# Performance work log

Measured on AMD Instinct MI355X. Metric: run time of the kernel, lower is better.

The kernel has to match this reference:

```python
import jax, jax.numpy as jnp
import numpy as np

B, S, D, H, L, DZ, POI, MAXP = 128, 512, 128, 4, 4, 128, 50000, 32
HD = D // H
EPS_LN = 1e-5

def layernorm(x, g, b):
    m = x.mean(-1, keepdims=True)
    v = ((x - m) ** 2).mean(-1, keepdims=True)
    return (x - m) * jax.lax.rsqrt(v + EPS_LN) * g + b

def setup_inputs() -> dict:
    key = jax.random.key(0)
    ks = iter(jax.random.split(key, 48))
    r = lambda shp, s=0.05: jax.random.normal(next(ks), shp, jnp.float32) * s
    return dict(
        d_t=jax.random.uniform(next(ks), (B, S), jnp.float32),
        d_l=jax.random.normal(next(ks), (B, S, 2), jnp.float32),
        d_emb=jax.random.randint(next(ks), (B, S), 0, POI),
        d_pad=jnp.zeros((B, S + 1), bool),
        num_pred=jax.random.randint(next(ks), (B,), 1, MAXP + 1),
        poi_table=r((POI, D), 0.02),
        W_time=r((D, 1)), W_space=r((D, 2)),
        agg_token=r((1, 1, D)),
        Wqkv=r((L, 3 * D, D), D ** -0.5), bqkv=jnp.zeros((L, 3 * D)),
        Wo=r((L, D, D), D ** -0.5), bo=jnp.zeros((L, D)),
        ln1_g=jnp.ones((L, D)), ln1_b=jnp.zeros((L, D)),
        W1=r((L, 2 * D, D), D ** -0.5), b1=jnp.zeros((L, 2 * D)),
        W2=r((L, D, 2 * D), (2 * D) ** -0.5), b2=jnp.zeros((L, D)),
        ln2_g=jnp.ones((L, D)), ln2_b=jnp.zeros((L, D)),
        Wg=r((DZ, D)), bg=jnp.zeros((DZ,)),
        Wt=r((DZ, D)), bt=jnp.zeros((DZ,)),
        gru_Wih=r((3 * D, D)), gru_Whh=r((3 * D, D)),
        gru_bih=jnp.zeros((3 * D,)), gru_bhh=jnp.zeros((3 * D,)),
        Wfc=r((1, D)), bfc=jnp.zeros((1,)),
    )

def reference(d_t, d_l, d_emb, d_pad, num_pred, poi_table, W_time, W_space, agg_token,
              Wqkv, bqkv, Wo, bo, ln1_g, ln1_b, W1, b1, W2, b2, ln2_g, ln2_b,
              Wg, bg, Wt, bt, gru_Wih, gru_Whh, gru_bih, gru_bhh, Wfc, bfc):
    # ---- Encoder: fused time/space/poi embeddings + agg token -> post-norm transformer stack ----
    t_emb = jnp.einsum('bs,d->bsd', d_t, W_time[:, 0])          # Linear(1, D, bias=False)
    c_emb = jnp.einsum('bsc,dc->bsd', d_l, W_space)             # Linear(2, D, bias=False)
    p_emb = poi_table[d_emb]                                    # [B,S,D]
    x = jnp.concatenate([t_emb + c_emb + p_emb,
                         jnp.broadcast_to(agg_token, (x_shape := (B, 1, D)))], axis=1)  # [B,S+1,D]
    T = S + 1
    neg = jnp.finfo(x.dtype).min
    for i in range(L):  # structurally distinct layers (post-norm, ReLU FFN, dropout=0)
        qkv = x @ Wqkv[i].T + bqkv[i]
        q, k, v = jnp.split(qkv, 3, axis=-1)
        hsplit = lambda t: t.reshape(B, T, H, HD).transpose(0, 2, 1, 3)
        q, k, v = hsplit(q), hsplit(k), hsplit(v)
        scores = jnp.einsum('bhqd,bhkd->bhqk', q, k) / jnp.sqrt(jnp.asarray(HD, x.dtype))
        scores = jnp.where(d_pad[:, None, None, :], neg, scores)
        attn = jax.nn.softmax(scores, axis=-1)
        o = jnp.einsum('bhqk,bhkd->bhqd', attn, v).transpose(0, 2, 1, 3).reshape(B, T, D)
        x = layernorm(x + o @ Wo[i].T + bo[i], ln1_g[i], ln1_b[i])
        ff = jax.nn.relu(x @ W1[i].T + b1[i]) @ W2[i].T + b2[i]
        x = layernorm(x + ff, ln2_g[i], ln2_b[i])
    ctx = x[:, -1, :]                                           # agg-token summary [B,D]
    gamma = ctx @ Wg.T + bg
    tau = jax.nn.softplus(ctx @ Wt.T + bt)

    # ---- DynamicTimeGenerator: batched GRUCell recurrence (input is the fixed zero init token) ----
    gi = jnp.zeros((1, D), ctx.dtype) @ gru_Wih.T + gru_bih      # [1,3D] input-side gates (x == 0)
    def step(h, _):
        gh = h @ gru_Whh.T + gru_bhh
        r = jax.nn.sigmoid(gi[:, :D] + gh[:, :D])
        z = jax.nn.sigmoid(gi[:, D:2 * D] + gh[:, D:2 * D])
        n = jnp.tanh(gi[:, 2 * D:] + r * gh[:, 2 * D:])
        h_new = (1.0 - z) * n + z * h
        delta = jax.nn.softplus(h_new @ Wfc.T + bfc)[:, 0]       # [B]
        return h_new, delta
    _, deltas = jax.lax.scan(step, ctx, None, length=MAXP)       # [MAXP, B]
    cum = jnp.cumsum(deltas, axis=0).T                           # [B, MAXP]
    last = jnp.take_along_axis(cum, (num_pred - 1)[:, None], axis=1)
    normed = cum / (last + 1e-6)
    valid = jnp.arange(MAXP)[None, :] < num_pred[:, None]
    times = jnp.zeros((B, MAXP + 2), ctx.dtype).at[:, 1:MAXP + 1].set(jnp.where(valid, normed, 0.0))
    times = times + jax.nn.one_hot(num_pred + 1, MAXP + 2, dtype=ctx.dtype)  # trailing 1.0 sentinel

    # ---- KL(q(z1)=N(gamma, tau^2) || N(0, I)) per kl_norm_norm ----
    a = jnp.sum(tau ** 2, -1, keepdims=True)
    b = jnp.sum(gamma ** 2, -1, keepdims=True)
    c = -2.0 * jnp.sum(jnp.log(tau), -1, keepdims=True)
    kl = 0.5 * (a + b + c - DZ)

    return jnp.concatenate([times, ctx, gamma, tau, kl], axis=-1)  # [B, MAXP+2+D+2*DZ+1]
```

## Files before the change

kernel.cpp:

```cpp
#include <hip/hip_runtime.h>

#define BB 128
#define SS 512
#define TT 513
#define DD 128
#define HH 4
#define LL 4
#define MM (BB*TT)

typedef __attribute__((ext_vector_type(4))) float f32x4;
typedef __attribute__((ext_vector_type(16))) float f32x16;
typedef __attribute__((ext_vector_type(8))) short short8;

__device__ __forceinline__ float b2f(ushort u){
  union { uint i; float f; } c; c.i = ((uint)u) << 16; return c.f;
}
__device__ __forceinline__ ushort f2b(float f){
  union { float f; uint i; } c; c.f = f;
  uint x = c.i;
  return (ushort)((x + 0x7fffu + ((x >> 16) & 1u)) >> 16);
}
union S8 { short8 v; ushort u[8]; };

__device__ __forceinline__ uint cvtpk(float lo, float hi){
  uint r;
  asm("v_cvt_pk_bf16_f32 %0, %1, %2" : "=v"(r) : "v"(lo), "v"(hi));
  return r;
}
__device__ __forceinline__ float fexp2(float x){
#if __has_builtin(__builtin_amdgcn_exp2f)
  return __builtin_amdgcn_exp2f(x);
#else
  return exp2f(x);
#endif
}

__global__ __launch_bounds__(256) void k_embed(
    const float* __restrict__ d_t, const float* __restrict__ d_l, const int* __restrict__ d_emb,
    const float* __restrict__ poi, const float* __restrict__ W_time, const float* __restrict__ W_space,
    const float* __restrict__ agg, ushort* __restrict__ xb)
{
  int gid = blockIdx.x*256 + threadIdx.x;
  if (gid >= MM*DD) return;
  int d = gid & 127;
  int m = gid >> 7;
  int b = m / TT, t = m % TT;
  float v;
  if (t == SS) v = agg[d];
  else {
    int bs = b*SS + t;
    v = d_t[bs]*W_time[d] + d_l[bs*2]*W_space[d*2] + d_l[bs*2+1]*W_space[d*2+1]
        + poi[(size_t)d_emb[bs]*DD + d];
  }
  xb[gid] = f2b(v);
}

__global__ __launch_bounds__(256) void k_f2b(const float* __restrict__ src, ushort* __restrict__ dst, int n){
  int i = blockIdx.x*256 + threadIdx.x;
  if (i < n) dst[i] = f2b(src[i]);
}

template<bool RELU, bool OUTB>
__global__ __launch_bounds__(256) void k_gemm(
  const ushort* __restrict__ A, const ushort* __restrict__ W,
  const float* __restrict__ bias, void* __restrict__ Cout,
  const int N, const int K)
{
  __shared__ __align__(16) ushort As[64*128], Ws[64*128];
  const int tid = threadIdx.x;
  const int m0 = blockIdx.x * 64, n0 = blockIdx.y * 64;
  const int l = tid & 63, wid = tid >> 6;
  const int wr = wid >> 1, wc = wid & 1;
  const int lr = l & 15, lg = l >> 4;
  f32x4 acc[2][2] = {};
  for (int kt = 0; kt < K; kt += 128){
    if (kt) __syncthreads();
    for (int i = tid; i < 1024; i += 256){
      const int row = i >> 4, ch = i & 15;
      const int bo_ = (ch*16) ^ ((row & 7) << 4);
      *(short8*)((char*)As + row*256 + bo_) = *(const short8*)&A[(size_t)(m0+row)*K + kt + ch*8];
      *(short8*)((char*)Ws + row*256 + bo_) = *(const short8*)&W[(size_t)(n0+row)*K + kt + ch*8];
    }
    __syncthreads();
    #pragma unroll
    for (int k0 = 0; k0 < 128; k0 += 32){
      const int sw = ((k0 + lg*8)*2) ^ ((lr & 7) << 4);
      short8 a0 = *(const short8*)((const char*)As + (wr*32+lr)*256 + sw);
      short8 a1 = *(const short8*)((const char*)As + (wr*32+16+lr)*256 + sw);
      short8 b0 = *(const short8*)((const char*)Ws + (wc*32+lr)*256 + sw);
      short8 b1 = *(const short8*)((const char*)Ws + (wc*32+16+lr)*256 + sw);
      acc[0][0] = __builtin_amdgcn_mfma_f32_16x16x32_bf16(a0, b0, acc[0][0], 0,0,0);
      acc[0][1] = __builtin_amdgcn_mfma_f32_16x16x32_bf16(a0, b1, acc[0][1], 0,0,0);
      acc[1][0] = __builtin_amdgcn_mfma_f32_16x16x32_bf16(a1, b0, acc[1][0], 0,0,0);
      acc[1][1] = __builtin_amdgcn_mfma_f32_16x16x32_bf16(a1, b1, acc[1][1], 0,0,0);
    }
  }
  #pragma unroll
  for (int i=0;i<2;i++)
  #pragma unroll
  for (int j=0;j<2;j++)
  #pragma unroll
  for (int r=0;r<4;r++){
    const int lm = wr*32 + i*16 + lg*4 + r;
    const int ln = wc*32 + j*16 + lr;
    const size_t idx = (size_t)(m0+lm)*N + (n0+ln);
    float v = acc[i][j][r] + bias[n0+ln];
    if (RELU) v = fmaxf(v, 0.f);
    if (OUTB) ((ushort*)Cout)[idx] = f2b(v);
    else ((float*)Cout)[idx] = v;
  }
}

__global__ __launch_bounds__(256) void k_gemm_ln(
  const ushort* __restrict__ A, const ushort* __restrict__ W,
  const float* __restrict__ bias, ushort* __restrict__ xb,
  const float* __restrict__ g, const float* __restrict__ bb, const int K)
{
  __shared__ __align__(16) ushort As[64*128], Ws[128*128];
  const int tid = threadIdx.x;
  const int m0 = blockIdx.x * 64;
  const int l = tid & 63, w = tid >> 6;
  const int lr = l & 15, lg = l >> 4;
  f32x4 acc[8] = {};
  for (int kt = 0; kt < K; kt += 128){
    if (kt) __syncthreads();
    for (int i = tid; i < 1024; i += 256){
      const int row = i >> 4, ch = i & 15;
      const int bo_ = (ch*16) ^ ((row & 7) << 4);
      *(short8*)((char*)As + row*256 + bo_) = *(const short8*)&A[(size_t)(m0+row)*K + kt + ch*8];
    }
    for (int i = tid; i < 2048; i += 256){
      const int row = i >> 4, ch = i & 15;
      const int bo_ = (ch*16) ^ ((row & 7) << 4);
      *(short8*)((char*)Ws + row*256 + bo_) = *(const short8*)&W[(size_t)row*K + kt + ch*8];
    }
    __syncthreads();
    #pragma unroll
    for (int k0 = 0; k0 < 128; k0 += 32){
      const int sw = ((k0 + lg*8)*2) ^ ((lr & 7) << 4);
      short8 a = *(const short8*)((const char*)As + (w*16+lr)*256 + sw);
      #pragma unroll
      for (int j=0;j<8;j++){
        short8 bf = *(const short8*)((const char*)Ws + (j*16+lr)*256 + sw);
        acc[j] = __builtin_amdgcn_mfma_f32_16x16x32_bf16(a, bf, acc[j], 0,0,0);
      }
    }
  }
  float biasj[8], gj[8], bj[8];
  #pragma unroll
  for (int j=0;j<8;j++){ biasj[j]=bias[j*16+lr]; gj[j]=g[j*16+lr]; bj[j]=bb[j*16+lr]; }
  #pragma unroll
  for (int r=0;r<4;r++){
    const size_t row = (size_t)(m0 + w*16 + lg*4 + r);
    float resid[8], s=0.f, sq=0.f;
    #pragma unroll
    for (int j=0;j<8;j++){
      float v = acc[j][r] + biasj[j];
      resid[j] = b2f(xb[row*128 + j*16 + lr]) + v;
      s += resid[j]; sq += resid[j]*resid[j];
    }
    #pragma unroll
    for (int off=1; off<16; off<<=1){ s += __shfl_xor(s,off,64); sq += __shfl_xor(sq,off,64); }
    const float mean = s*(1.f/128.f);
    const float var  = fmaxf(sq*(1.f/128.f) - mean*mean, 0.f);
    const float rstd = rsqrtf(var + 1e-5f);
    #pragma unroll
    for (int j=0;j<8;j++){
      float o = (resid[j]-mean)*rstd*gj[j] + bj[j];
      xb[row*128 + j*16 + lr] = f2b(o);
    }
  }
}

#define VSTRIDE 544
#define NEGM 30000.f
#define MFMA32(a,b,c) __builtin_amdgcn_mfma_f32_32x32x16_bf16(a,b,c,0,0,0)

__global__ __launch_bounds__(512) void k_attn(const ushort* __restrict__ qkv, ushort* __restrict__ ao)
{
  __shared__ __align__(16) ushort KL[VSTRIDE*32];
  __shared__ __align__(16) ushort VT[32*VSTRIDE];
  const int tid = threadIdx.x;
  const int b = blockIdx.x >> 2, h = blockIdx.x & 3;
  const size_t base = (size_t)b*TT*384 + h*32;
  union { short4 v; ushort u[4]; } sv;
  for (int i = tid; i < 8*VSTRIDE; i += 512){
    int t = i >> 3, dc = (i & 7)*4;
    sv.u[0]=0; sv.u[1]=0; sv.u[2]=0; sv.u[3]=0;
    if (t < TT) sv.v = *(const short4*)&qkv[base + (size_t)t*384 + 128 + dc];
    *(short4*)((char*)KL + ((t*64 + dc*2) ^ ((t&7)<<4))) = sv.v;
  }
  for (int i = tid; i < 8*VSTRIDE; i += 512){
    int t = i >> 3, dc = (i & 7)*4;
    sv.u[0]=0; sv.u[1]=0; sv.u[2]=0; sv.u[3]=0;
    if (t < TT) sv.v = *(const short4*)&qkv[base + (size_t)t*384 + 256 + dc];
    #pragma unroll
    for (int e=0;e<4;e++){
      int d = dc + e;
      *(ushort*)((char*)VT + ((d*1088 + t*2) ^ ((d&7)<<4))) = sv.u[e];
    }
  }
  __syncthreads();
  const int l = tid & 63, w = tid >> 6;
  const int lq = l & 31, hi = l >> 5;
  const float qscale = 0.25503486341f;
  const int krow = (lq & 3) | ((lq & 4) << 1) | ((lq & 8) >> 1) | (lq & 16);
  f32x16 cinit;
  #pragma unroll
  for (int r=0;r<16;r++) cinit[r] = -40.f;

  for (int qi = 0; qi < 3; qi++){
    const int qb = w + qi*8;
    if (qb >= 17) break;
    const int q0 = qb*32;
    int qrow = q0 + lq; if (qrow > SS) qrow = SS;
    S8 qa, qf0, qf1;
    qa.v = *(const short8*)&qkv[base + (size_t)qrow*384 + hi*8];
    #pragma unroll
    for (int j=0;j<8;j++) qf0.u[j] = f2b(b2f(qa.u[j]) * qscale);
    qa.v = *(const short8*)&qkv[base + (size_t)qrow*384 + 16 + hi*8];
    #pragma unroll
    for (int j=0;j<8;j++) qf1.u[j] = f2b(b2f(qa.u[j]) * qscale);

    float rsl = 0.f;
    f32x16 acc = {};
    int t0 = 0;
    for (int kb = 0; kb < 17; kb++, t0 += 32){
      const int trow = t0 + krow;
      short8 kc0 = *(const short8*)((const char*)KL + ((trow*64 + hi*16)      ^ ((trow&7)<<4)));
      short8 kc1 = *(const short8*)((const char*)KL + ((trow*64 + 32 + hi*16) ^ ((trow&7)<<4)));
      f32x16 s = MFMA32(kc0, qf0.v, cinit);
      s = MFMA32(kc1, qf1.v, s);
      if (t0 + 32 > TT){
        #pragma unroll
        for (int r=0;r<16;r++){
          const int key = t0 + (r&7) + 8*hi + 16*(r>>3);
          if (key >= TT) s[r] = -NEGM;
        }
      }
      float p[16];
      #pragma unroll
      for (int r=0;r<16;r++){ p[r] = fexp2(s[r]); rsl += p[r]; }
      union { short8 v; uint u[4]; } pa0, pa1;
      #pragma unroll
      for (int wd=0; wd<4; wd++){
        pa0.u[wd] = cvtpk(p[2*wd],   p[2*wd+1]);
        pa1.u[wd] = cvtpk(p[8+2*wd], p[8+2*wd+1]);
      }
      short8 v0 = *(const short8*)((const char*)VT + (((lq*1088) + (t0 + hi*8)*2)      ^ ((lq&7)<<4)));
      short8 v1 = *(const short8*)((const char*)VT + (((lq*1088) + (t0 + 16 + hi*8)*2) ^ ((lq&7)<<4)));
      acc = MFMA32(v0, pa0.v, acc);
      acc = MFMA32(v1, pa1.v, acc);
    }
    rsl += __shfl_xor(rsl, 32, 64);
    if (q0 + lq < TT){
      const float inv = 1.f / rsl;
      ushort* orow = ao + ((size_t)(b*TT + q0 + lq))*DD + h*32;
      #pragma unroll
      for (int r=0;r<16;r++){
        const int d = (r&3) + 8*(r>>2) + 4*hi;
        orow[d] = f2b(acc[r]*inv);
      }
    }
  }
}

__global__ __launch_bounds__(256) void k_ctx(
    const ushort* __restrict__ xb, const float* __restrict__ Wg, const float* __restrict__ bg,
    const float* __restrict__ Wt, const float* __restrict__ bt,
    float* __restrict__ out, float* __restrict__ ctxws)
{
  __shared__ float cs[128];
  const int b = blockIdx.x, tid = threadIdx.x;
  const ushort* xr = &xb[((size_t)b*TT + SS)*128];
  if (tid < 128){
    float v = b2f(xr[tid]);
    cs[tid] = v;
    out[(size_t)b*419 + 34 + tid] = v;
    ctxws[b*128 + tid] = v;
  }
  __syncthreads();
  const int j = tid & 127;
  const float* Wrow = (tid < 128) ? &Wg[(size_t)j*128] : &Wt[(size_t)j*128];
  float acc = 0.f;
  #pragma unroll 8
  for (int d=0; d<128; d+=4){
    float4 wv = *(const float4*)&Wrow[d];
    acc += cs[d]*wv.x + cs[d+1]*wv.y + cs[d+2]*wv.z + cs[d+3]*wv.w;
  }
  if (tid < 128){
    out[(size_t)b*419 + 162 + j] = acc + bg[j];
  } else {
    float tv = acc + bt[j];
    float sp = fmaxf(tv, 0.f) + log1pf(__expf(-fabsf(tv)));
    out[(size_t)b*419 + 290 + j] = sp;
  }
}

__global__ __launch_bounds__(384, 1) void k_gru(
    const float* __restrict__ ctx, const float* __restrict__ Whh,
    const float* __restrict__ bih, const float* __restrict__ bhh,
    const float* __restrict__ Wfc, const float* __restrict__ bfc,
    float* __restrict__ deltas)
{
  __shared__ float hs[128], gh[384], red[2];
  const int b = blockIdx.x, tid = threadIdx.x;
  if (tid < 128) hs[tid] = ctx[b*128 + tid];
  float4 wreg[32];
  const float4* wp = (const float4*)&Whh[(size_t)tid*128];
  #pragma unroll
  for (int d=0; d<32; d++) wreg[d] = wp[d];
  const float bhh_t = bhh[tid];
  float bih0=0.f, bih1=0.f, bih2=0.f, wfc_t=0.f;
  if (tid < 128){ bih0=bih[tid]; bih1=bih[128+tid]; bih2=bih[256+tid]; wfc_t=Wfc[tid]; }
  const float bfc0 = bfc[0];
  for (int step=0; step<32; step++){
    __syncthreads();
    float acc = bhh_t;
    #pragma unroll
    for (int d=0; d<32; d++){
      acc += hs[4*d]*wreg[d].x + hs[4*d+1]*wreg[d].y + hs[4*d+2]*wreg[d].z + hs[4*d+3]*wreg[d].w;
    }
    gh[tid] = acc;
    __syncthreads();
    if (tid < 128){
      float r = 1.f/(1.f + __expf(-(bih0 + gh[tid])));
      float z = 1.f/(1.f + __expf(-(bih1 + gh[128+tid])));
      float n = tanhf(bih2 + r*gh[256+tid]);
      float hn = (1.f - z)*n + z*hs[tid];
      hs[tid] = hn;
      float pv = hn * wfc_t;
      #pragma unroll
      for (int off=1; off<64; off<<=1) pv += __shfl_xor(pv, off, 64);
      if ((tid & 63) == 0) red[tid >> 6] = pv;
    }
    __syncthreads();
    if (tid == 0){
      float dv = red[0] + red[1] + bfc0;
      deltas[b*32 + step] = fmaxf(dv, 0.f) + log1pf(__expf(-fabsf(dv)));
    }
  }
}

__global__ __launch_bounds__(64) void k_final(
    const float* __restrict__ deltas, const int* __restrict__ num_pred,
    float* __restrict__ out)
{
  const int b = blockIdx.x, l = threadIdx.x;
  float d = (l < 32) ? deltas[b*32 + l] : 0.f;
  float c = d;
  #pragma unroll
  for (int off=1; off<32; off<<=1){
    float t = __shfl_up(c, off, 64);
    if (l >= off) c += t;
  }
  const int np = num_pred[b];
  float last = __shfl(c, np-1, 64);
  float denom = last + 1e-6f;
  float cjm = __shfl(c, (l==0 ? 0 : l-1), 64);
  float val = 0.f;
  if (l >= 1 && l <= 32 && (l-1) < np) val = cjm / denom;
  if (l == np + 1) val += 1.f;
  if (l < 34) out[(size_t)b*419 + l] = val;
  float ta = 0.f, tb = 0.f, tc = 0.f;
  for (int z = l; z < 128; z += 64){
    float ga = out[(size_t)b*419 + 162 + z];
    float tu = fmaxf(out[(size_t)b*419 + 290 + z], 1e-35f);
    ta += tu*tu; tb += ga*ga; tc += -2.f*logf(tu);
  }
  float v = ta + tb + tc;
  #pragma unroll
  for (int off=1; off<64; off<<=1) v += __shfl_xor(v, off, 64);
  if (l == 0) out[(size_t)b*419 + 418] = 0.5f*(v - 128.f);
}

extern "C" void kernel_launch(void* const* d_in, const int* in_sizes, int n_in,
                              void* d_out, int out_size, void* d_ws, size_t ws_size,
                              hipStream_t stream)
{
  (void)in_sizes; (void)n_in; (void)out_size; (void)ws_size;
  const float* d_t    = (const float*)d_in[0];
  const float* d_l    = (const float*)d_in[1];
  const int*   d_emb  = (const int*)  d_in[2];
  const int*   numprd = (const int*)  d_in[4];
  const float* poi    = (const float*)d_in[5];
  const float* W_time = (const float*)d_in[6];
  const float* W_space= (const float*)d_in[7];
  const float* agg    = (const float*)d_in[8];
  const float* Wqkv   = (const float*)d_in[9];
  const float* bqkv   = (const float*)d_in[10];
  const float* Wo     = (const float*)d_in[11];
  const float* bo     = (const float*)d_in[12];
  const float* ln1g   = (const float*)d_in[13];
  const float* ln1b   = (const float*)d_in[14];
  const float* W1     = (const float*)d_in[15];
  const float* b1     = (const float*)d_in[16];
  const float* W2     = (const float*)d_in[17];
  const float* b2     = (const float*)d_in[18];
  const float* ln2g   = (const float*)d_in[19];
  const float* ln2b   = (const float*)d_in[20];
  const float* Wg     = (const float*)d_in[21];
  const float* bg     = (const float*)d_in[22];
  const float* Wt     = (const float*)d_in[23];
  const float* bt     = (const float*)d_in[24];
  const float* Whh    = (const float*)d_in[26];
  const float* bih    = (const float*)d_in[27];
  const float* bhh    = (const float*)d_in[28];
  const float* Wfc    = (const float*)d_in[29];
  const float* bfc    = (const float*)d_in[30];
  float* out = (float*)d_out;

  char* ws = (char*)d_ws;
  size_t off = 0;
  auto alloc = [&](size_t bytes){ size_t o = off; off += (bytes + 255) & ~(size_t)255; return o; };
  ushort* xb    = (ushort*)(ws + alloc((size_t)MM*128*2));
  ushort* qkv   = (ushort*)(ws + alloc((size_t)MM*384*2));
  ushort* aob   = (ushort*)(ws + alloc((size_t)MM*128*2));
  ushort* hb    = (ushort*)(ws + alloc((size_t)MM*256*2));
  ushort* wqkvb = (ushort*)(ws + alloc((size_t)LL*384*128*2));
  ushort* wob   = (ushort*)(ws + alloc((size_t)LL*128*128*2));
  ushort* w1b   = (ushort*)(ws + alloc((size_t)LL*256*128*2));
  ushort* w2b   = (ushort*)(ws + alloc((size_t)LL*128*256*2));
  float*  ctxws = (float*) (ws + alloc(128*128*4));
  float*  deltas= (float*) (ws + alloc(128*32*4));

  k_f2b<<<(LL*384*128+255)/256,256,0,stream>>>(Wqkv, wqkvb, LL*384*128);
  k_f2b<<<(LL*128*128+255)/256,256,0,stream>>>(Wo,   wob,   LL*128*128);
  k_f2b<<<(LL*256*128+255)/256,256,0,stream>>>(W1,   w1b,   LL*256*128);
  k_f2b<<<(LL*128*256+255)/256,256,0,stream>>>(W2,   w2b,   LL*128*256);
  k_embed<<<(MM*DD)/256,256,0,stream>>>(d_t, d_l, d_emb, poi, W_time, W_space, agg, xb);

  for (int li = 0; li < LL; li++){
    dim3 gq(MM/64, 6);
    k_gemm<false,true><<<gq,256,0,stream>>>(xb, wqkvb + li*384*128, bqkv + li*384, qkv, 384, 128);
    k_attn<<<BB*HH,512,0,stream>>>(qkv, aob);
    k_gemm_ln<<<MM/64,256,0,stream>>>(aob, wob + li*128*128, bo + li*128, xb,
                                      ln1g + li*128, ln1b + li*128, 128);
    dim3 gf(MM/64, 4);
    k_gemm<true,true><<<gf,256,0,stream>>>(xb, w1b + li*256*128, b1 + li*256, hb, 256, 128);
    k_gemm_ln<<<MM/64,256,0,stream>>>(hb, w2b + li*128*256, b2 + li*128, xb,
                                      ln2g + li*128, ln2b + li*128, 256);
  }

  k_ctx<<<128,256,0,stream>>>(xb, Wg, bg, Wt, bt, out, ctxws);
  k_gru<<<128,384,0,stream>>>(ctxws, Whh, bih, bhh, Wfc, bfc, deltas);
  k_final<<<128,64,0,stream>>>(deltas, numprd, out);
}
```

Before: 594.6 us.

## Loop all N tiles per GEMM block and batch GRU steps with bf16 MFMA

The QKV and FFN1 GEMMs now launch one block per 64-row M tile. Each block loads its A tile into shared memory once and loops over every N tile, instead of reloading A for each N block in a 2D grid. Separately, the GRU recurrence now handles 16 batch rows per block using bf16 MFMA with Whh kept in registers, replacing one fp32 FMA block per batch row. This cuts the number of serial per-step kernels' worth of work. It trades grid parallelism for reuse, and the GRU hidden state is now rounded to bf16 each step, which may change accuracy.

```diff
diff --git a/kernel.cpp b/kernel.cpp
--- a/kernel.cpp
+++ b/kernel.cpp
@@ -60,28 +60,31 @@
   if (i < n) dst[i] = f2b(src[i]);
 }
 
-template<bool RELU, bool OUTB>
-__global__ __launch_bounds__(256) void k_gemm(
+template<bool RELU>
+__global__ __launch_bounds__(256) void k_gemm2(
   const ushort* __restrict__ A, const ushort* __restrict__ W,
-  const float* __restrict__ bias, void* __restrict__ Cout,
-  const int N, const int K)
+  const float* __restrict__ bias, ushort* __restrict__ Cout, const int N)
 {
   __shared__ __align__(16) ushort As[64*128], Ws[64*128];
   const int tid = threadIdx.x;
-  const int m0 = blockIdx.x * 64, n0 = blockIdx.y * 64;
+  const int m0 = blockIdx.x * 64;
   const int l = tid & 63, wid = tid >> 6;
   const int wr = wid >> 1, wc = wid & 1;
   const int lr = l & 15, lg = l >> 4;
-  f32x4 acc[2][2] = {};
-  for (int kt = 0; kt < K; kt += 128){
-    if (kt) __syncthreads();
+  for (int i = tid; i < 1024; i += 256){
+    const int row = i >> 4, ch = i & 15;
+    const int bo_ = (ch*16) ^ ((row & 7) << 4);
+    *(short8*)((char*)As + row*256 + bo_) = *(const short8*)&A[(size_t)(m0+row)*128 + ch*8];
+  }
+  for (int n0 = 0; n0 < N; n0 += 64){
+    if (n0) __syncthreads();
     for (int i = tid; i < 1024; i += 256){
       const int row = i >> 4, ch = i & 15;
       const int bo_ = (ch*16) ^ ((row & 7) << 4);
-      *(short8*)((char*)As + row*256 + bo_) = *(const short8*)&A[(size_t)(m0+row)*K + kt + ch*8];
-      *(short8*)((char*)Ws + row*256 + bo_) = *(const short8*)&W[(size_t)(n0+row)*K + kt + ch*8];
+      *(short8*)((char*)Ws + row*256 + bo_) = *(const short8*)&W[(size_t)(n0+row)*128 + ch*8];
     }
     __syncthreads();
+    f32x4 acc[2][2] = {};
     #pragma unroll
     for (int k0 = 0; k0 < 128; k0 += 32){
       const int sw = ((k0 + lg*8)*2) ^ ((lr & 7) << 4);
@@ -94,20 +97,18 @@
       acc[1][0] = __builtin_amdgcn_mfma_f32_16x16x32_bf16(a1, b0, acc[1][0], 0,0,0);
       acc[1][1] = __builtin_amdgcn_mfma_f32_16x16x32_bf16(a1, b1, acc[1][1], 0,0,0);
     }
-  }
-  #pragma unroll
-  for (int i=0;i<2;i++)
-  #pragma unroll
-  for (int j=0;j<2;j++)
-  #pragma unroll
-  for (int r=0;r<4;r++){
-    const int lm = wr*32 + i*16 + lg*4 + r;
-    const int ln = wc*32 + j*16 + lr;
-    const size_t idx = (size_t)(m0+lm)*N + (n0+ln);
-    float v = acc[i][j][r] + bias[n0+ln];
-    if (RELU) v = fmaxf(v, 0.f);
-    if (OUTB) ((ushort*)Cout)[idx] = f2b(v);
-    else ((float*)Cout)[idx] = v;
+    #pragma unroll
+    for (int i=0;i<2;i++)
+    #pragma unroll
+    for (int j=0;j<2;j++)
+    #pragma unroll
+    for (int r=0;r<4;r++){
+      const int lm = wr*32 + i*16 + lg*4 + r;
+      const int ln = n0 + wc*32 + j*16 + lr;
+      float v = acc[i][j][r] + bias[ln];
+      if (RELU) v = fmaxf(v, 0.f);
+      Cout[(size_t)(m0+lm)*N + ln] = f2b(v);
+    }
   }
 }
 
@@ -297,48 +298,95 @@
   }
 }
 
-__global__ __launch_bounds__(384, 1) void k_gru(
-    const float* __restrict__ ctx, const float* __restrict__ Whh,
+#define GB 16
+__global__ __launch_bounds__(512, 1) void k_gru(
+    const float* __restrict__ ctx, const ushort* __restrict__ whh_b,
     const float* __restrict__ bih, const float* __restrict__ bhh,
     const float* __restrict__ Wfc, const float* __restrict__ bfc,
     float* __restrict__ deltas)
 {
-  __shared__ float hs[128], gh[384], red[2];
-  const int b = blockIdx.x, tid = threadIdx.x;
-  if (tid < 128) hs[tid] = ctx[b*128 + tid];
-  float4 wreg[32];
-  const float4* wp = (const float4*)&Whh[(size_t)tid*128];
-  #pragma unroll
-  for (int d=0; d<32; d++) wreg[d] = wp[d];
-  const float bhh_t = bhh[tid];
-  float bih0=0.f, bih1=0.f, bih2=0.f, wfc_t=0.f;
-  if (tid < 128){ bih0=bih[tid]; bih1=bih[128+tid]; bih2=bih[256+tid]; wfc_t=Wfc[tid]; }
+  __shared__ __align__(16) uint hb2[16*68];
+  __shared__ __align__(16) float ghs[16*388];
+  __shared__ float red[GB];
+  const int tid = threadIdx.x;
+  const int b0 = blockIdx.x * GB;
+  const int l = tid & 63, w = tid >> 6;
+  const int lr = l & 15, lg = l >> 4;
+  short8 wb[3][4];
+  #pragma unroll
+  for (int t=0;t<3;t++){
+    const int nrow = 16*w + t*128 + lr;
+    #pragma unroll
+    for (int kc=0;kc<4;kc++)
+      wb[t][kc] = *(const short8*)&whh_b[(size_t)nrow*128 + kc*32 + lg*8];
+  }
+  const int ab = tid >> 5, ad = (tid & 31) * 4;
+  float bi0a[4], bi1a[4], bi2a[4], bh0a[4], bh1a[4], bh2a[4], wfa[4];
+  #pragma unroll
+  for (int j=0;j<4;j++){
+    bi0a[j]=bih[ad+j]; bi1a[j]=bih[128+ad+j]; bi2a[j]=bih[256+ad+j];
+    bh0a[j]=bhh[ad+j]; bh1a[j]=bhh[128+ad+j]; bh2a[j]=bhh[256+ad+j];
+    wfa[j]=Wfc[ad+j];
+  }
   const float bfc0 = bfc[0];
+  for (int i = tid; i < 16*64; i += 512){
+    const int bb = i >> 6, j = i & 63;
+    const float h0 = ctx[(size_t)(b0+bb)*128 + 2*j];
+    const float h1 = ctx[(size_t)(b0+bb)*128 + 2*j + 1];
+    hb2[bb*68 + j] = (uint)f2b(h0) | (((uint)f2b(h1)) << 16);
+  }
   for (int step=0; step<32; step++){
     __syncthreads();
-    float acc = bhh_t;
-    #pragma unroll
-    for (int d=0; d<32; d++){
-      acc += hs[4*d]*wreg[d].x + hs[4*d+1]*wreg[d].y + hs[4*d+2]*wreg[d].z + hs[4*d+3]*wreg[d].w;
-    }
-    gh[tid] = acc;
+    if (step && tid < GB){
+      const float dv = red[tid] + bfc0;
+      deltas[(size_t)(b0+tid)*32 + (step-1)] = fmaxf(dv,0.f) + log1pf(__expf(-fabsf(dv)));
+    }
+    union { short8 v; uint4 q; } af[4];
+    #pragma unroll
+    for (int kc=0;kc<4;kc++)
+      af[kc].q = *(const uint4*)&hb2[lr*68 + kc*16 + lg*4];
+    f32x4 acc0 = {}, acc1 = {}, acc2 = {};
+    #pragma unroll
+    for (int kc=0;kc<4;kc++){
+      acc0 = __builtin_amdgcn_mfma_f32_16x16x32_bf16(af[kc].v, wb[0][kc], acc0, 0,0,0);
+      acc1 = __builtin_amdgcn_mfma_f32_16x16x32_bf16(af[kc].v, wb[1][kc], acc1, 0,0,0);
+      acc2 = __builtin_amdgcn_mfma_f32_16x16x32_bf16(af[kc].v, wb[2][kc], acc2, 0,0,0);
+    }
+    #pragma unroll
+    for (int r=0;r<4;r++){
+      ghs[(lg*4+r)*388 + 16*w + lr]       = acc0[r];
+      ghs[(lg*4+r)*388 + 16*w + 128 + lr] = acc1[r];
+      ghs[(lg*4+r)*388 + 16*w + 256 + lr] = acc2[r];
+    }
     __syncthreads();
-    if (tid < 128){
-      float r = 1.f/(1.f + __expf(-(bih0 + gh[tid])));
-      float z = 1.f/(1.f + __expf(-(bih1 + gh[128+tid])));
-      float n = tanhf(bih2 + r*gh[256+tid]);
-      float hn = (1.f - z)*n + z*hs[tid];
-      hs[tid] = hn;
-      float pv = hn * wfc_t;
-      #pragma unroll
-      for (int off=1; off<64; off<<=1) pv += __shfl_xor(pv, off, 64);
-      if ((tid & 63) == 0) red[tid >> 6] = pv;
-    }
-    __syncthreads();
-    if (tid == 0){
-      float dv = red[0] + red[1] + bfc0;
-      deltas[b*32 + step] = fmaxf(dv, 0.f) + log1pf(__expf(-fabsf(dv)));
-    }
+    float4 gr = *(const float4*)&ghs[ab*388 + ad];
+    float4 gz = *(const float4*)&ghs[ab*388 + 128 + ad];
+    float4 gn = *(const float4*)&ghs[ab*388 + 256 + ad];
+    const float grs[4] = {gr.x,gr.y,gr.z,gr.w};
+    const float gzs[4] = {gz.x,gz.y,gz.z,gz.w};
+    const float gns[4] = {gn.x,gn.y,gn.z,gn.w};
+    const uint hp0 = hb2[ab*68 + (ad>>1)], hp1 = hb2[ab*68 + (ad>>1) + 1];
+    const float h[4] = { b2f((ushort)hp0), b2f((ushort)(hp0>>16)),
+                         b2f((ushort)hp1), b2f((ushort)(hp1>>16)) };
+    float hn[4], pv = 0.f;
+    #pragma unroll
+    for (int j=0;j<4;j++){
+      const float rr = 1.f/(1.f + __expf(-(bi0a[j] + bh0a[j] + grs[j])));
+      const float zz = 1.f/(1.f + __expf(-(bi1a[j] + bh1a[j] + gzs[j])));
+      const float nn = tanhf(bi2a[j] + rr*(gns[j] + bh2a[j]));
+      hn[j] = (1.f - zz)*nn + zz*h[j];
+      pv += hn[j]*wfa[j];
+    }
+    hb2[ab*68 + (ad>>1)]     = (uint)f2b(hn[0]) | (((uint)f2b(hn[1])) << 16);
+    hb2[ab*68 + (ad>>1) + 1] = (uint)f2b(hn[2]) | (((uint)f2b(hn[3])) << 16);
+    #pragma unroll
+    for (int off=1; off<32; off<<=1) pv += __shfl_xor(pv, off, 64);
+    if ((tid & 31) == 0) red[ab] = pv;
+  }
+  __syncthreads();
+  if (tid < GB){
+    const float dv = red[tid] + bfc0;
+    deltas[(size_t)(b0+tid)*32 + 31] = fmaxf(dv,0.f) + log1pf(__expf(-fabsf(dv)));
   }
 }
 
@@ -421,6 +469,7 @@
   ushort* wob   = (ushort*)(ws + alloc((size_t)LL*128*128*2));
   ushort* w1b   = (ushort*)(ws + alloc((size_t)LL*256*128*2));
   ushort* w2b   = (ushort*)(ws + alloc((size_t)LL*128*256*2));
+  ushort* whhb  = (ushort*)(ws + alloc((size_t)384*128*2));
   float*  ctxws = (float*) (ws + alloc(128*128*4));
   float*  deltas= (float*) (ws + alloc(128*32*4));
 
@@ -428,21 +477,20 @@
   k_f2b<<<(LL*128*128+255)/256,256,0,stream>>>(Wo,   wob,   LL*128*128);
   k_f2b<<<(LL*256*128+255)/256,256,0,stream>>>(W1,   w1b,   LL*256*128);
   k_f2b<<<(LL*128*256+255)/256,256,0,stream>>>(W2,   w2b,   LL*128*256);
+  k_f2b<<<(384*128+255)/256,256,0,stream>>>(Whh, whhb, 384*128);
   k_embed<<<(MM*DD)/256,256,0,stream>>>(d_t, d_l, d_emb, poi, W_time, W_space, agg, xb);
 
   for (int li = 0; li < LL; li++){
-    dim3 gq(MM/64, 6);
-    k_gemm<false,true><<<gq,256,0,stream>>>(xb, wqkvb + li*384*128, bqkv + li*384, qkv, 384, 128);
+    k_gemm2<false><<<MM/64,256,0,stream>>>(xb, wqkvb + li*384*128, bqkv + li*384, qkv, 384);
     k_attn<<<BB*HH,512,0,stream>>>(qkv, aob);
     k_gemm_ln<<<MM/64,256,0,stream>>>(aob, wob + li*128*128, bo + li*128, xb,
                                       ln1g + li*128, ln1b + li*128, 128);
-    dim3 gf(MM/64, 4);
-    k_gemm<true,true><<<gf,256,0,stream>>>(xb, w1b + li*256*128, b1 + li*256, hb, 256, 128);
+    k_gemm2<true><<<MM/64,256,0,stream>>>(xb, w1b + li*256*128, b1 + li*256, hb, 256);
     k_gemm_ln<<<MM/64,256,0,stream>>>(hb, w2b + li*128*256, b2 + li*128, xb,
                                       ln2g + li*128, ln2b + li*128, 256);
   }
 
   k_ctx<<<128,256,0,stream>>>(xb, Wg, bg, Wt, bt, out, ctxws);
-  k_gru<<<128,384,0,stream>>>(ctxws, Whh, bih, bhh, Wfc, bfc, deltas);
+  k_gru<<<8,512,0,stream>>>(ctxws, whhb, bih, bhh, Wfc, bfc, deltas);
   k_final<<<128,64,0,stream>>>(deltas, numprd, out);
 }
```

After: 594.4 us. About the same (-0.0%).
